# Optimization experiments

Measured on AMD Instinct MI355X. Metric: run time of the kernel, lower is better.

## Reference

```python
import jax, jax.numpy as jnp
import numpy as np

LAYER_VEC = [2000, 200, 100, 10]
EN_DIMS = [(2000, 200), (200, 100), (100, 10)]      # (num_in, num_out) per encoder FC_layer
DE_DIMS = [(10, 100), (100, 200), (200, 2000)]      # decoder is reversed
EN_SIZES = [ni * no + no for ni, no in EN_DIMS]     # [400200, 20100, 1010] -> 421310
DE_SIZES = [ni * no + no for ni, no in DE_DIMS]     # [1100, 20200, 402000] -> 423300
ACT_VEC = ['linear', 'tanh', 'linear']              # ['linear'] + (len-3)*[activation] + ['linear']


def _hyper(mu, W0, b0, W1, b1, W2, b2):
    # nn.Sequential: Linear -> tanh -> Linear -> tanh -> Linear (depth_hyper=2)
    h = jnp.tanh(mu @ W0.T + b0)
    h = jnp.tanh(h @ W1.T + b1)
    return h @ W2.T + b2  # [B, param_size]


def _fc_layer(x, p, num_in, num_out):
    # FC_layer.forward: per-sample weight matvec + bias
    B = x.shape[0]
    w = p[:, :num_out * num_in].reshape(B, num_out, num_in)
    b = p[:, num_out * num_in:]
    return jnp.einsum('ab,acb->ac', x, w) + b


def _act(x, name):
    return jnp.tanh(x) if name == 'tanh' else x


def _run_stack(data, params, dims, sizes):
    cut = 0
    for (ni, no), sz, a in zip(dims, sizes, ACT_VEC):
        data = _act(_fc_layer(data, params[:, cut:cut + sz], ni, no), a)
        cut += sz
    return data


def setup_inputs() -> dict:
    key = jax.random.key(0)
    ks = jax.random.split(key, 16)
    B, NS, W = 64, 4, 64
    EN_P, DE_P = sum(EN_SIZES), sum(DE_SIZES)
    f32 = jnp.float32
    inp = {
        'z':  jax.random.normal(ks[0], (B, LAYER_VEC[0]), f32),
        'mu': jax.random.normal(ks[1], (B, NS), f32),
        'en_W0': jax.random.normal(ks[2], (W, NS), f32) / np.sqrt(NS),
        'en_b0': jnp.zeros((W,), f32),
        'en_W1': jax.random.normal(ks[3], (W, W), f32) / np.sqrt(W),
        'en_b1': jnp.zeros((W,), f32),
        'en_W2': jax.random.normal(ks[4], (EN_P, W), f32) * 0.01,
        'en_b2': jnp.zeros((EN_P,), f32),
        'de_W0': jax.random.normal(ks[5], (W, NS), f32) / np.sqrt(NS),
        'de_b0': jnp.zeros((W,), f32),
        'de_W1': jax.random.normal(ks[6], (W, W), f32) / np.sqrt(W),
        'de_b1': jnp.zeros((W,), f32),
        'de_W2': jax.random.normal(ks[7], (DE_P, W), f32) * 0.01,
        'de_b2': jnp.zeros((DE_P,), f32),
    }
    return inp


def reference(z, mu, en_W0, en_b0, en_W1, en_b1, en_W2, en_b2,
              de_W0, de_b0, de_W1, de_b1, de_W2, de_b2):
    # encode
    p_en = _hyper(mu, en_W0, en_b0, en_W1, en_b1, en_W2, en_b2)
    x = _run_stack(z, p_en, EN_DIMS, EN_SIZES)
    # decode
    p_de = _hyper(mu, de_W0, de_b0, de_W1, de_b1, de_W2, de_b2)
    z_reconst = _run_stack(x, p_de, DE_DIMS, DE_SIZES)
    return (z_reconst, x)
```

## Files before the change

kernel.cpp:

```cpp
#include <hip/hip_runtime.h>


__global__ __launch_bounds__(256) void prep_kernel(
    const float* __restrict__ z, const float* __restrict__ mu,
    const float* __restrict__ enW0, const float* __restrict__ enb0,
    const float* __restrict__ enW1, const float* __restrict__ enb1,
    const float* __restrict__ deW0, const float* __restrict__ deb0,
    const float* __restrict__ deW1, const float* __restrict__ deb1,
    float* __restrict__ zT, float* __restrict__ hen, float* __restrict__ hde)
{
    __shared__ float tile[64 * 65];
    __shared__ float h0s[4][64];
    const int bid  = blockIdx.x;
    const int lane = threadIdx.x & 63;
    const int g    = threadIdx.x >> 6;

    if (bid < 32) {
        const int t0 = bid * 64;
        for (int bb = g; bb < 64; bb += 4) {
            int i = t0 + lane;
            tile[bb * 65 + lane] = (i < 2000) ? z[bb * 2000 + i] : 0.f;
        }
        __syncthreads();
        for (int ii = g; ii < 64; ii += 4) {
            int i = t0 + ii;
            if (i < 2000) zT[i * 64 + lane] = tile[lane * 65 + ii];
        }
    } else {
        const int task  = (bid - 32) * 4 + g;
        const int which = task >> 6;
        const int b     = task & 63;
        const float* W0 = which ? deW0 : enW0;
        const float* b0 = which ? deb0 : enb0;
        const float* W1 = which ? deW1 : enW1;
        const float* b1 = which ? deb1 : enb1;
        float* hout     = which ? hde : hen;
        const int j = lane;
        float m0 = mu[b * 4 + 0], m1 = mu[b * 4 + 1], m2 = mu[b * 4 + 2], m3 = mu[b * 4 + 3];
        float v = tanhf(m0 * W0[j * 4 + 0] + m1 * W0[j * 4 + 1] +
                        m2 * W0[j * 4 + 2] + m3 * W0[j * 4 + 3] + b0[j]);
        h0s[g][j] = v;
        __syncthreads();
        float a = b1[j];
        const float* W1r = W1 + j * 64;
        #pragma unroll 8
        for (int k = 0; k < 64; ++k) a = fmaf(h0s[g][k], W1r[k], a);
        hout[b * 64 + j] = tanhf(a);
    }
}

template <int NI, int NO, int NSPLIT, bool TANH, bool ATOMIC>
__global__ __launch_bounds__(256, 2) void fc_kernel(
    const float* __restrict__ xT,
    const float* __restrict__ h,
    const float* __restrict__ W2,
    const float* __restrict__ b2,
    float* __restrict__ yT)
{
    __shared__ float R[2][64 * 64];
    __shared__ float xbs[256];
    const int lane = threadIdx.x & 63;
    const int wave = __builtin_amdgcn_readfirstlane(threadIdx.x >> 6);
    const int o = blockIdx.x / NSPLIT;
    const int s = blockIdx.x % NSPLIT;
    constexpr int CH = NI / NSPLIT;
    const int i0 = s * CH;
    const int iend = i0 + CH;

    const float* __restrict__ Wbase = W2 + (size_t)o * NI * 64;
    const float* __restrict__ b2w   = b2 + (size_t)o * NI;

    float acc[64];
    #pragma unroll
    for (int b = 0; b < 64; ++b) acc[b] = 0.f;
    float xb_acc = 0.f;

    #pragma unroll 2
    for (int i = i0 + wave; i < iend; i += 4) {
        float w = Wbase[(size_t)i * 64 + lane];
        float xv_l = xT[i * 64 + lane];
        xb_acc = fmaf(xv_l, b2w[i], xb_acc);
        const float4* xr = (const float4*)(xT + i * 64);
        #pragma unroll
        for (int q = 0; q < 16; ++q) {
            float4 xv = xr[q];
            acc[4 * q + 0] = fmaf(xv.x, w, acc[4 * q + 0]);
            acc[4 * q + 1] = fmaf(xv.y, w, acc[4 * q + 1]);
            acc[4 * q + 2] = fmaf(xv.z, w, acc[4 * q + 2]);
            acc[4 * q + 3] = fmaf(xv.w, w, acc[4 * q + 3]);
        }
    }

    xbs[wave * 64 + lane] = xb_acc;

    if (wave == 1) {
        #pragma unroll
        for (int b = 0; b < 64; ++b) R[0][b * 64 + lane] = acc[b];
    } else if (wave == 3) {
        #pragma unroll
        for (int b = 0; b < 64; ++b) R[1][b * 64 + lane] = acc[b];
    }
    __syncthreads();
    if (wave == 0) {
        #pragma unroll
        for (int b = 0; b < 64; ++b) acc[b] += R[0][b * 64 + lane];
    } else if (wave == 2) {
        #pragma unroll
        for (int b = 0; b < 64; ++b) acc[b] += R[1][b * 64 + lane];
    }
    __syncthreads();
    if (wave == 0) {
        #pragma unroll
        for (int b = 0; b < 64; ++b) R[0][b * 64 + lane] = acc[b];
    } else if (wave == 2) {
        #pragma unroll
        for (int b = 0; b < 64; ++b) R[1][b * 64 + lane] = acc[b];
    }
    __syncthreads();

    float wsel = 0.f;
    if (!ATOMIC || s == 0) wsel = W2[((size_t)NO * NI + o) * 64 + lane];
    float myv = 0.f;
    #pragma unroll
    for (int j = 0; j < 16; ++j) {
        int b = wave * 16 + j;
        float t = R[0][b * 64 + lane] + R[1][b * 64 + lane];
        float v = (t + wsel) * h[b * 64 + lane];
        #pragma unroll
        for (int m = 32; m >= 1; m >>= 1) v += __shfl_xor(v, m, 64);
        if (lane == j) myv = v;
    }
    if (lane < 16) {
        int b = wave * 16 + lane;
        float xbt = xbs[b] + xbs[64 + b] + xbs[128 + b] + xbs[192 + b];
        float out = myv + xbt;
        if (!ATOMIC || s == 0) out += b2[(size_t)NO * NI + o];
        if (TANH) out = tanhf(out);
        if (ATOMIC) atomicAdd(&yT[o * 64 + b], out);
        else        yT[o * 64 + b] = out;
    }
}

__global__ __launch_bounds__(256) void final_kernel(
    const float* __restrict__ d3,
    const float* __restrict__ y3,
    float* __restrict__ out)
{
    int t = blockIdx.x * 256 + threadIdx.x;
    if (t < 128000) {
        int b = t / 2000, oo = t - b * 2000;
        out[t] = d3[oo * 64 + b];
    } else if (t < 128640) {
        int u = t - 128000;
        int b = u / 10, oo = u - b * 10;
        out[t] = y3[oo * 64 + b];
    }
}

extern "C" void kernel_launch(void* const* d_in, const int* in_sizes, int n_in,
                              void* d_out, int out_size, void* d_ws, size_t ws_size,
                              hipStream_t stream)
{
    const float* z    = (const float*)d_in[0];
    const float* mu   = (const float*)d_in[1];
    const float* enW0 = (const float*)d_in[2];
    const float* enb0 = (const float*)d_in[3];
    const float* enW1 = (const float*)d_in[4];
    const float* enb1 = (const float*)d_in[5];
    const float* enW2 = (const float*)d_in[6];
    const float* enb2 = (const float*)d_in[7];
    const float* deW0 = (const float*)d_in[8];
    const float* deb0 = (const float*)d_in[9];
    const float* deW1 = (const float*)d_in[10];
    const float* deb1 = (const float*)d_in[11];
    const float* deW2 = (const float*)d_in[12];
    const float* deb2 = (const float*)d_in[13];

    float* ws  = (float*)d_ws;
    float* zT  = ws;
    float* hen = zT + 128000;
    float* hde = hen + 4096;
    float* y1  = hde + 4096;
    float* y2  = y1 + 200 * 64;
    float* y3  = y2 + 100 * 64;
    float* d1  = y3 + 10 * 64;
    float* d2  = d1 + 100 * 64;
    float* d3  = d2 + 200 * 64;
    float* out = (float*)d_out;

    hipMemsetAsync(y1, 0, 200 * 64 * sizeof(float), stream);
    prep_kernel<<<64, 256, 0, stream>>>(z, mu, enW0, enb0, enW1, enb1,
                                        deW0, deb0, deW1, deb1, zT, hen, hde);
    fc_kernel<2000, 200, 8, false, true ><<<1600, 256, 0, stream>>>(zT, hen, enW2, enb2, y1);
    fc_kernel< 200, 100, 1, true,  false><<< 100, 256, 0, stream>>>(y1, hen, enW2 + (size_t)400200 * 64, enb2 + 400200, y2);
    fc_kernel< 100,  10, 1, false, false><<<  10, 256, 0, stream>>>(y2, hen, enW2 + (size_t)420300 * 64, enb2 + 420300, y3);
    fc_kernel<  10, 100, 1, false, false><<< 100, 256, 0, stream>>>(y3, hde, deW2, deb2, d1);
    fc_kernel< 100, 200, 1, true,  false><<< 200, 256, 0, stream>>>(d1, hde, deW2 + (size_t)1100 * 64, deb2 + 1100, d2);
    fc_kernel< 200, 2000, 1, false, false><<<2000, 256, 0, stream>>>(d2, hde, deW2 + (size_t)21300 * 64, deb2 + 21300, d3);

    final_kernel<<<(128640 + 255) / 256, 256, 0, stream>>>(d3, y3, out);
}
```

Before: 381.9 us.

## Split batch across waves instead of input dim to drop LDS reduction

Each wave now owns 16 batch columns and iterates over the whole input chunk, instead of each wave covering a quarter of the input rows for all 64 batch entries. This removes the 64-entry accumulator array and the multi-stage shared-memory cross-wave reduction with its three barriers, which lowers register pressure and LDS traffic. In exchange, all four waves load the same weight row, so redundant global or cache loads of W rise fourfold per block. The large encoder layer is also split into 10 chunks instead of 8.

```diff
diff --git a/kernel.cpp b/kernel.cpp
--- a/kernel.cpp
+++ b/kernel.cpp
@@ -50,90 +50,72 @@
 }
 
 template <int NI, int NO, int NSPLIT, bool TANH, bool ATOMIC>
-__global__ __launch_bounds__(256, 2) void fc_kernel(
+__global__ __launch_bounds__(256) void fc_kernel(
     const float* __restrict__ xT,
     const float* __restrict__ h,
     const float* __restrict__ W2,
     const float* __restrict__ b2,
     float* __restrict__ yT)
 {
-    __shared__ float R[2][64 * 64];
-    __shared__ float xbs[256];
+    __shared__ float xbs[64];
     const int lane = threadIdx.x & 63;
     const int wave = __builtin_amdgcn_readfirstlane(threadIdx.x >> 6);
     const int o = blockIdx.x / NSPLIT;
-    const int s = blockIdx.x % NSPLIT;
+    const int s = blockIdx.x - o * NSPLIT;
     constexpr int CH = NI / NSPLIT;
     const int i0 = s * CH;
-    const int iend = i0 + CH;
 
-    const float* __restrict__ Wbase = W2 + (size_t)o * NI * 64;
-    const float* __restrict__ b2w   = b2 + (size_t)o * NI;
+    const float* __restrict__ Wp  = W2 + ((size_t)o * NI + i0) * 64 + lane;
+    const float* __restrict__ xp  = xT + i0 * 64;
+    const float* __restrict__ b2w = b2 + (size_t)o * NI + i0;
 
-    float acc[64];
+    float acc[16];
     #pragma unroll
-    for (int b = 0; b < 64; ++b) acc[b] = 0.f;
+    for (int j = 0; j < 16; ++j) acc[j] = 0.f;
     float xb_acc = 0.f;
 
-    #pragma unroll 2
-    for (int i = i0 + wave; i < iend; i += 4) {
-        float w = Wbase[(size_t)i * 64 + lane];
-        float xv_l = xT[i * 64 + lane];
-        xb_acc = fmaf(xv_l, b2w[i], xb_acc);
-        const float4* xr = (const float4*)(xT + i * 64);
-        #pragma unroll
-        for (int q = 0; q < 16; ++q) {
-            float4 xv = xr[q];
-            acc[4 * q + 0] = fmaf(xv.x, w, acc[4 * q + 0]);
-            acc[4 * q + 1] = fmaf(xv.y, w, acc[4 * q + 1]);
-            acc[4 * q + 2] = fmaf(xv.z, w, acc[4 * q + 2]);
-            acc[4 * q + 3] = fmaf(xv.w, w, acc[4 * q + 3]);
-        }
+    #pragma unroll 4
+    for (int i = 0; i < CH; ++i) {
+        float w = Wp[(size_t)i * 64];
+        if (wave == 0)
+            xb_acc = fmaf(xp[i * 64 + lane], b2w[i], xb_acc);
+        const float4* xr = (const float4*)(xp + i * 64 + wave * 16);
+        float4 x0 = xr[0], x1 = xr[1], x2 = xr[2], x3 = xr[3];
+        acc[ 0] = fmaf(x0.x, w, acc[ 0]);
+        acc[ 1] = fmaf(x0.y, w, acc[ 1]);
+        acc[ 2] = fmaf(x0.z, w, acc[ 2]);
+        acc[ 3] = fmaf(x0.w, w, acc[ 3]);
+        acc[ 4] = fmaf(x1.x, w, acc[ 4]);
+        acc[ 5] = fmaf(x1.y, w, acc[ 5]);
+        acc[ 6] = fmaf(x1.z, w, acc[ 6]);
+        acc[ 7] = fmaf(x1.w, w, acc[ 7]);
+        acc[ 8] = fmaf(x2.x, w, acc[ 8]);
+        acc[ 9] = fmaf(x2.y, w, acc[ 9]);
+        acc[10] = fmaf(x2.z, w, acc[10]);
+        acc[11] = fmaf(x2.w, w, acc[11]);
+        acc[12] = fmaf(x3.x, w, acc[12]);
+        acc[13] = fmaf(x3.y, w, acc[13]);
+        acc[14] = fmaf(x3.z, w, acc[14]);
+        acc[15] = fmaf(x3.w, w, acc[15]);
     }
 
-    xbs[wave * 64 + lane] = xb_acc;
+    if (wave == 0) xbs[lane] = xb_acc;
 
-    if (wave == 1) {
-        #pragma unroll
-        for (int b = 0; b < 64; ++b) R[0][b * 64 + lane] = acc[b];
-    } else if (wave == 3) {
-        #pragma unroll
-        for (int b = 0; b < 64; ++b) R[1][b * 64 + lane] = acc[b];
-    }
-    __syncthreads();
-    if (wave == 0) {
-        #pragma unroll
-        for (int b = 0; b < 64; ++b) acc[b] += R[0][b * 64 + lane];
-    } else if (wave == 2) {
-        #pragma unroll
-        for (int b = 0; b < 64; ++b) acc[b] += R[1][b * 64 + lane];
-    }
-    __syncthreads();
-    if (wave == 0) {
-        #pragma unroll
-        for (int b = 0; b < 64; ++b) R[0][b * 64 + lane] = acc[b];
-    } else if (wave == 2) {
-        #pragma unroll
-        for (int b = 0; b < 64; ++b) R[1][b * 64 + lane] = acc[b];
-    }
-    __syncthreads();
-
-    float wsel = 0.f;
-    if (!ATOMIC || s == 0) wsel = W2[((size_t)NO * NI + o) * 64 + lane];
+    float wb = 0.f;
+    if (!ATOMIC || s == 0) wb = W2[((size_t)NO * NI + o) * 64 + lane];
     float myv = 0.f;
     #pragma unroll
     for (int j = 0; j < 16; ++j) {
         int b = wave * 16 + j;
-        float t = R[0][b * 64 + lane] + R[1][b * 64 + lane];
-        float v = (t + wsel) * h[b * 64 + lane];
+        float v = (acc[j] + wb) * h[b * 64 + lane];
         #pragma unroll
         for (int m = 32; m >= 1; m >>= 1) v += __shfl_xor(v, m, 64);
         if (lane == j) myv = v;
     }
+    __syncthreads();
     if (lane < 16) {
         int b = wave * 16 + lane;
-        float xbt = xbs[b] + xbs[64 + b] + xbs[128 + b] + xbs[192 + b];
-        float out = myv + xbt;
+        float out = myv + xbs[b];
         if (!ATOMIC || s == 0) out += b2[(size_t)NO * NI + o];
         if (TANH) out = tanhf(out);
         if (ATOMIC) atomicAdd(&yT[o * 64 + b], out);
@@ -191,11 +173,11 @@
     hipMemsetAsync(y1, 0, 200 * 64 * sizeof(float), stream);
     prep_kernel<<<64, 256, 0, stream>>>(z, mu, enW0, enb0, enW1, enb1,
                                         deW0, deb0, deW1, deb1, zT, hen, hde);
-    fc_kernel<2000, 200, 8, false, true ><<<1600, 256, 0, stream>>>(zT, hen, enW2, enb2, y1);
-    fc_kernel< 200, 100, 1, true,  false><<< 100, 256, 0, stream>>>(y1, hen, enW2 + (size_t)400200 * 64, enb2 + 400200, y2);
-    fc_kernel< 100,  10, 1, false, false><<<  10, 256, 0, stream>>>(y2, hen, enW2 + (size_t)420300 * 64, enb2 + 420300, y3);
-    fc_kernel<  10, 100, 1, false, false><<< 100, 256, 0, stream>>>(y3, hde, deW2, deb2, d1);
-    fc_kernel< 100, 200, 1, true,  false><<< 200, 256, 0, stream>>>(d1, hde, deW2 + (size_t)1100 * 64, deb2 + 1100, d2);
+    fc_kernel<2000, 200, 10, false, true ><<<2000, 256, 0, stream>>>(zT, hen, enW2, enb2, y1);
+    fc_kernel< 200, 100,  1, true,  false><<< 100, 256, 0, stream>>>(y1, hen, enW2 + (size_t)400200 * 64, enb2 + 400200, y2);
+    fc_kernel< 100,  10,  1, false, false><<<  10, 256, 0, stream>>>(y2, hen, enW2 + (size_t)420300 * 64, enb2 + 420300, y3);
+    fc_kernel<  10, 100,  1, false, false><<< 100, 256, 0, stream>>>(y3, hde, deW2, deb2, d1);
+    fc_kernel< 100, 200,  1, true,  false><<< 200, 256, 0, stream>>>(d1, hde, deW2 + (size_t)1100 * 64, deb2 + 1100, d2);
     fc_kernel< 200, 2000, 1, false, false><<<2000, 256, 0, stream>>>(d2, hde, deW2 + (size_t)21300 * 64, deb2 + 21300, d3);
 
     final_kernel<<<(128640 + 255) / 256, 256, 0, stream>>>(d3, y3, out);
```

Result: slower. 563.5 us (+47.6%).
